# Kernel optimization log

Measured on AMD Instinct MI355X. Metric: run time of the kernel, lower is better.

## Reference

```python
import jax, jax.numpy as jnp
import numpy as np

NL, B, L1, L2, D = 4, 64, 256, 256, 1024
LOGIT_SCALE = 1.0
BN_EPS = 1e-8


def setup_inputs() -> dict:
    key = jax.random.key(0)
    k1, k2, k3, k4, k5, k6 = jax.random.split(key, 6)
    reps1 = jax.random.normal(k1, (NL, B, L1, D), dtype=jnp.float32)
    reps2 = jax.random.normal(k2, (NL, B, L2, D), dtype=jnp.float32)
    len1 = jax.random.randint(k3, (B,), 1, L1 + 1)
    len2 = jax.random.randint(k4, (B,), 1, L2 + 1)
    w = jax.random.normal(k5, (1, NL), dtype=jnp.float32) * 0.1
    b = jax.random.normal(k6, (1,), dtype=jnp.float32) * 0.1
    return {"reps1": reps1, "reps2": reps2, "len1": len1, "len2": len2, "w": w, "b": b}


def reference(reps1, reps2, len1, len2, w, b):
    # reps: (NL, B, L, D) hidden states of selected layers, already (B-major per layer)
    neg = jnp.finfo(reps1.dtype).min
    # cosine-normalize along feature dim
    h1 = reps1 / jnp.linalg.norm(reps1, axis=-1, keepdims=True)
    h2 = reps2 / jnp.linalg.norm(reps2, axis=-1, keepdims=True)
    # similarity matrices for all layers at once: (NL, B, L1, L2)
    dots = jnp.einsum("lbid,lbjd->lbij", h1, h2)
    # ragged validity masks
    mask1 = jnp.arange(L1)[None, :] < len1[:, None]  # (B, L1)
    mask2 = jnp.arange(L2)[None, :] < len2[:, None]  # (B, L2)
    n1 = len1.astype(dots.dtype)
    n2 = len2.astype(dots.dtype)
    # max over valid rows i, mean over valid cols j  -> s1 (NL, B)
    max_i = jnp.max(jnp.where(mask1[None, :, :, None], dots, neg), axis=2)  # (NL,B,L2)
    s1 = jnp.sum(jnp.where(mask2[None], max_i, 0.0), axis=2) / n2[None]
    # max over valid cols j, mean over valid rows i  -> s2 (NL, B)
    max_j = jnp.max(jnp.where(mask2[None, :, None, :], dots, neg), axis=3)  # (NL,B,L1)
    s2 = jnp.sum(jnp.where(mask1[None], max_j, 0.0), axis=2) / n1[None]
    # harmonic mean (F1)
    feat = (2.0 * s1 * s2 / (s1 + s2)).T  # (B, NL)
    # BatchNorm1d(affine=False), training mode: batch stats, biased variance
    mean = jnp.mean(feat, axis=0, keepdims=True)
    var = jnp.mean((feat - mean) ** 2, axis=0, keepdims=True)
    feat = (feat - mean) / jnp.sqrt(var + BN_EPS)
    # final linear head + logit scale -> (B,)
    return LOGIT_SCALE * (feat @ w.T + b)[:, 0]
```

## Files before the change

kernel.cpp:

```cpp
#include <hip/hip_runtime.h>

#define NLAYERS 4
#define BATCH   64
#define LEN1    256
#define LEN2    256
#define DIM     1024
#define BKK     32
#define NKT     (DIM / BKK)

typedef _Float16 f16x8 __attribute__((ext_vector_type(8)));
typedef float    f32x4 __attribute__((ext_vector_type(4)));

typedef __attribute__((address_space(1))) const void gas_void;
typedef __attribute__((address_space(3))) void       las_void;

__device__ __forceinline__ void dma16(const float* g, float* l) {
  __builtin_amdgcn_global_load_lds((gas_void*)g, (las_void*)l, 16, 0, 0);
}

__device__ __forceinline__ void block_bar() {
  asm volatile("" ::: "memory");
  __builtin_amdgcn_s_barrier();
  asm volatile("" ::: "memory");
}

#define WAITVM(N) asm volatile("s_waitcnt vmcnt(" #N ")" ::: "memory")

__global__ __launch_bounds__(1024, 4)
void bs_main(const float* __restrict__ reps1, const float* __restrict__ reps2,
             const int* __restrict__ len1, const int* __restrict__ len2,
             float* __restrict__ feat) {
  __shared__ float Af[2][LEN1 * BKK];
  __shared__ float Bf[2][LEN2 * BKK];
  __shared__ float ssq1[LEN1];
  __shared__ float ssq2[LEN2];
  __shared__ float rowp[LEN1][4];
  __shared__ float colp[LEN2][4];
  __shared__ float redbuf[32];

  const int bid = blockIdx.x;
  const int nl  = bid >> 6;
  const int bb  = bid & 63;
  const float* gA = reps1 + (size_t)bid * LEN1 * DIM;
  const float* gB = reps2 + (size_t)bid * LEN2 * DIM;

  const int tid  = threadIdx.x;
  const int lane = tid & 63;
  const int wid  = tid >> 6;
  const int wm   = wid >> 2;
  const int wn   = wid & 3;
  const int li   = lane & 15;
  const int lh   = lane >> 4;

  f32x4 acc[4][4];
  #pragma unroll
  for (int a = 0; a < 4; ++a)
    #pragma unroll
    for (int c = 0; c < 4; ++c) acc[a][c] = 0.0f;

  const int r0  = tid >> 3;
  const int ch0 = tid & 7;
  const int sc0 = (ch0 ^ (r0 & 7)) << 2;
  const int sc1 = (ch0 ^ ((r0 + 128) & 7)) << 2;

  float pssqA0 = 0.f, pssqA1 = 0.f, pssqB0 = 0.f, pssqB1 = 0.f;

  auto stage = [&](int kt, int buf) {
    const int col = kt * BKK;
    dma16(gA + (size_t)r0 * DIM + col + sc0,          &Af[buf][tid * 4]);
    dma16(gB + (size_t)r0 * DIM + col + sc0,          &Bf[buf][tid * 4]);
    dma16(gA + (size_t)(r0 + 128) * DIM + col + sc1,  &Af[buf][(tid + 1024) * 4]);
    dma16(gB + (size_t)(r0 + 128) * DIM + col + sc1,  &Bf[buf][(tid + 1024) * 4]);
  };

  stage(0, 0);

  #pragma unroll 1
  for (int kt = 0; kt < NKT; ++kt) {
    const int cur = kt & 1;
    if (kt + 1 < NKT) {
      stage(kt + 1, cur ^ 1);
      WAITVM(4);
    } else {
      WAITVM(0);
    }
    block_bar();

    const float* Ac = Af[cur];
    const float* Bc = Bf[cur];

    {
      const float4 a0 = *(const float4*)&Ac[tid * 4];
      const float4 a1 = *(const float4*)&Ac[(tid + 1024) * 4];
      const float4 b0 = *(const float4*)&Bc[tid * 4];
      const float4 b1 = *(const float4*)&Bc[(tid + 1024) * 4];
      pssqA0 += a0.x*a0.x + a0.y*a0.y + a0.z*a0.z + a0.w*a0.w;
      pssqA1 += a1.x*a1.x + a1.y*a1.y + a1.z*a1.z + a1.w*a1.w;
      pssqB0 += b0.x*b0.x + b0.y*b0.y + b0.z*b0.z + b0.w*b0.w;
      pssqB1 += b1.x*b1.x + b1.y*b1.y + b1.z*b1.z + b1.w*b1.w;
    }

    f16x8 af[4];
    #pragma unroll
    for (int fm = 0; fm < 4; ++fm) {
      const int r = wm * 64 + fm * 16 + li;
      const float4 x0 = *(const float4*)&Ac[r * BKK + ((((lh << 1)    ) ^ (r & 7)) << 2)];
      const float4 x1 = *(const float4*)&Ac[r * BKK + ((((lh << 1) | 1) ^ (r & 7)) << 2)];
      f16x8 h;
      h[0] = (_Float16)x0.x; h[1] = (_Float16)x0.y; h[2] = (_Float16)x0.z; h[3] = (_Float16)x0.w;
      h[4] = (_Float16)x1.x; h[5] = (_Float16)x1.y; h[6] = (_Float16)x1.z; h[7] = (_Float16)x1.w;
      af[fm] = h;
    }
    #pragma unroll
    for (int fn = 0; fn < 4; ++fn) {
      const int r = wn * 64 + fn * 16 + li;
      const float4 y0 = *(const float4*)&Bc[r * BKK + ((((lh << 1)    ) ^ (r & 7)) << 2)];
      const float4 y1 = *(const float4*)&Bc[r * BKK + ((((lh << 1) | 1) ^ (r & 7)) << 2)];
      f16x8 bh;
      bh[0] = (_Float16)y0.x; bh[1] = (_Float16)y0.y; bh[2] = (_Float16)y0.z; bh[3] = (_Float16)y0.w;
      bh[4] = (_Float16)y1.x; bh[5] = (_Float16)y1.y; bh[6] = (_Float16)y1.z; bh[7] = (_Float16)y1.w;
      #pragma unroll
      for (int fm = 0; fm < 4; ++fm)
        acc[fm][fn] = __builtin_amdgcn_mfma_f32_16x16x32_f16(af[fm], bh, acc[fm][fn], 0, 0, 0);
    }

    block_bar();
  }

  #pragma unroll
  for (int m = 1; m <= 4; m <<= 1) {
    pssqA0 += __shfl_xor(pssqA0, m, 64);
    pssqA1 += __shfl_xor(pssqA1, m, 64);
    pssqB0 += __shfl_xor(pssqB0, m, 64);
    pssqB1 += __shfl_xor(pssqB1, m, 64);
  }
  if ((lane & 7) == 0) {
    ssq1[r0] = pssqA0;  ssq1[r0 + 128] = pssqA1;
    ssq2[r0] = pssqB0;  ssq2[r0 + 128] = pssqB1;
  }
  __syncthreads();
  if (tid < 256)       ssq1[tid] = 1.0f / sqrtf(ssq1[tid]);
  else if (tid < 512)  ssq2[tid - 256] = 1.0f / sqrtf(ssq2[tid - 256]);
  __syncthreads();

  const int n1 = len1[bb];
  const int n2 = len2[bb];

  float rn2v[4];
  bool  jv[4];
  #pragma unroll
  for (int fn = 0; fn < 4; ++fn) {
    const int j = wn * 64 + fn * 16 + li;
    rn2v[fn] = ssq2[j];
    jv[fn]   = (j < n2);
  }
  float rn1v[4][4];
  bool  iv[4][4];
  #pragma unroll
  for (int fm = 0; fm < 4; ++fm)
    #pragma unroll
    for (int rg = 0; rg < 4; ++rg) {
      const int i = wm * 64 + fm * 16 + lh * 4 + rg;
      rn1v[fm][rg] = ssq1[i];
      iv[fm][rg]   = (i < n1);
    }

  const float NEG = -3.402823466e38f;
  float rowm[4][4];
  float colm[4];
  #pragma unroll
  for (int fm = 0; fm < 4; ++fm)
    #pragma unroll
    for (int rg = 0; rg < 4; ++rg) rowm[fm][rg] = NEG;
  #pragma unroll
  for (int fn = 0; fn < 4; ++fn) colm[fn] = NEG;

  #pragma unroll
  for (int fm = 0; fm < 4; ++fm)
    #pragma unroll
    for (int fn = 0; fn < 4; ++fn)
      #pragma unroll
      for (int rg = 0; rg < 4; ++rg) {
        const float v = acc[fm][fn][rg] * rn1v[fm][rg] * rn2v[fn];
        if (jv[fn] && v > rowm[fm][rg]) rowm[fm][rg] = v;
        if (iv[fm][rg] && v > colm[fn]) colm[fn] = v;
      }

  #pragma unroll
  for (int m = 1; m <= 8; m <<= 1)
    #pragma unroll
    for (int fm = 0; fm < 4; ++fm)
      #pragma unroll
      for (int rg = 0; rg < 4; ++rg) {
        const float o = __shfl_xor(rowm[fm][rg], m, 64);
        rowm[fm][rg] = fmaxf(rowm[fm][rg], o);
      }
  #pragma unroll
  for (int m = 16; m <= 32; m <<= 1)
    #pragma unroll
    for (int fn = 0; fn < 4; ++fn) {
      const float o = __shfl_xor(colm[fn], m, 64);
      colm[fn] = fmaxf(colm[fn], o);
    }

  if (li == 0)
    #pragma unroll
    for (int fm = 0; fm < 4; ++fm)
      #pragma unroll
      for (int rg = 0; rg < 4; ++rg)
        rowp[wm * 64 + fm * 16 + lh * 4 + rg][wn] = rowm[fm][rg];
  if (lh == 0)
    #pragma unroll
    for (int fn = 0; fn < 4; ++fn)
      colp[wn * 64 + fn * 16 + li][wm] = colm[fn];
  __syncthreads();

  float c1 = 0.f, c2 = 0.f;
  if (tid < 256) {
    const float rm = fmaxf(fmaxf(rowp[tid][0], rowp[tid][1]),
                           fmaxf(rowp[tid][2], rowp[tid][3]));
    if (tid < n1) c2 = rm;
    const float cm = fmaxf(fmaxf(colp[tid][0], colp[tid][1]),
                           fmaxf(colp[tid][2], colp[tid][3]));
    if (tid < n2) c1 = cm;
  }
  #pragma unroll
  for (int m = 1; m <= 32; m <<= 1) {
    c1 += __shfl_xor(c1, m, 64);
    c2 += __shfl_xor(c2, m, 64);
  }
  if (lane == 0) {
    redbuf[wid]      = c1;
    redbuf[16 + wid] = c2;
  }
  __syncthreads();
  if (tid == 0) {
    float s1s = 0.f, s2s = 0.f;
    #pragma unroll
    for (int i = 0; i < 16; ++i) { s1s += redbuf[i]; s2s += redbuf[16 + i]; }
    const float s1 = s1s / (float)n2;
    const float s2 = s2s / (float)n1;
    feat[bb * NLAYERS + nl] = 2.0f * s1 * s2 / (s1 + s2);
  }
}

__global__ void bs_head(const float* __restrict__ feat, const float* __restrict__ w,
                        const float* __restrict__ bias, float* __restrict__ out) {
  __shared__ float lds[NLAYERS][BATCH];
  const int tid = threadIdx.x;
  const int nl  = tid >> 6;
  const int b   = tid & 63;

  const float x = feat[b * NLAYERS + nl];
  float s = x;
  #pragma unroll
  for (int m = 1; m <= 32; m <<= 1) s += __shfl_xor(s, m, 64);
  const float mean = s / 64.0f;
  const float d = x - mean;
  float v = d * d;
  #pragma unroll
  for (int m = 1; m <= 32; m <<= 1) v += __shfl_xor(v, m, 64);
  const float var = v / 64.0f;
  const float y = d / sqrtf(var + 1e-8f);

  lds[nl][b] = y * w[nl];
  __syncthreads();
  if (tid < 64)
    out[tid] = lds[0][tid] + lds[1][tid] + lds[2][tid] + lds[3][tid] + bias[0];
}

extern "C" void kernel_launch(void* const* d_in, const int* in_sizes, int n_in,
                              void* d_out, int out_size, void* d_ws, size_t ws_size,
                              hipStream_t stream) {
  const float* reps1 = (const float*)d_in[0];
  const float* reps2 = (const float*)d_in[1];
  const int*   len1  = (const int*)d_in[2];
  const int*   len2  = (const int*)d_in[3];
  const float* w     = (const float*)d_in[4];
  const float* bias  = (const float*)d_in[5];
  float* feat = (float*)d_ws;

  bs_main<<<NLAYERS * BATCH, 1024, 0, stream>>>(reps1, reps2, len1, len2, feat);
  bs_head<<<1, 256, 0, stream>>>(feat, w, bias, (float*)d_out);
}
```

Baseline: 127.7 us.

## Use 4-stage pipeline with 16-wide K tiles and 16x16x16 MFMA

Halves the K tile width to 16, moves from double to quad buffering with three tiles in flight, and switches to the 16x16x16 f16 MFMA with 4-element fragments. Each thread now issues two DMA loads per stage instead of four, and the swizzle and sum-of-squares reduction are adapted to 4 chunks per row. The goal is deeper memory latency hiding at the same LDS footprint, at the cost of twice as many barriers and loop iterations and a lower-throughput MFMA variant.

Result: slower. 148.4 us (+16.2%).

```diff
diff --git a/kernel.cpp b/kernel.cpp
--- a/kernel.cpp
+++ b/kernel.cpp
@@ -5,10 +5,11 @@
 #define LEN1    256
 #define LEN2    256
 #define DIM     1024
-#define BKK     32
+#define BKK     16
 #define NKT     (DIM / BKK)
-
-typedef _Float16 f16x8 __attribute__((ext_vector_type(8)));
+#define NBUF    4
+
+typedef _Float16 f16x4 __attribute__((ext_vector_type(4)));
 typedef float    f32x4 __attribute__((ext_vector_type(4)));
 
 typedef __attribute__((address_space(1))) const void gas_void;
@@ -30,8 +31,8 @@
 void bs_main(const float* __restrict__ reps1, const float* __restrict__ reps2,
              const int* __restrict__ len1, const int* __restrict__ len2,
              float* __restrict__ feat) {
-  __shared__ float Af[2][LEN1 * BKK];
-  __shared__ float Bf[2][LEN2 * BKK];
+  __shared__ float Af[NBUF][LEN1 * BKK];
+  __shared__ float Bf[NBUF][LEN2 * BKK];
   __shared__ float ssq1[LEN1];
   __shared__ float ssq2[LEN2];
   __shared__ float rowp[LEN1][4];
@@ -58,32 +59,29 @@
     #pragma unroll
     for (int c = 0; c < 4; ++c) acc[a][c] = 0.0f;
 
-  const int r0  = tid >> 3;
-  const int ch0 = tid & 7;
-  const int sc0 = (ch0 ^ (r0 & 7)) << 2;
-  const int sc1 = (ch0 ^ ((r0 + 128) & 7)) << 2;
-
-  float pssqA0 = 0.f, pssqA1 = 0.f, pssqB0 = 0.f, pssqB1 = 0.f;
+  const int rS  = tid >> 2;
+  const int chS = tid & 3;
+  const int sc  = (chS ^ (rS & 3)) << 2;
+
+  float pssqA = 0.f, pssqB = 0.f;
 
   auto stage = [&](int kt, int buf) {
-    const int col = kt * BKK;
-    dma16(gA + (size_t)r0 * DIM + col + sc0,          &Af[buf][tid * 4]);
-    dma16(gB + (size_t)r0 * DIM + col + sc0,          &Bf[buf][tid * 4]);
-    dma16(gA + (size_t)(r0 + 128) * DIM + col + sc1,  &Af[buf][(tid + 1024) * 4]);
-    dma16(gB + (size_t)(r0 + 128) * DIM + col + sc1,  &Bf[buf][(tid + 1024) * 4]);
+    const int col = kt * BKK + sc;
+    dma16(gA + (size_t)rS * DIM + col, &Af[buf][tid * 4]);
+    dma16(gB + (size_t)rS * DIM + col, &Bf[buf][tid * 4]);
   };
 
   stage(0, 0);
+  stage(1, 1);
+  stage(2, 2);
 
   #pragma unroll 1
   for (int kt = 0; kt < NKT; ++kt) {
-    const int cur = kt & 1;
-    if (kt + 1 < NKT) {
-      stage(kt + 1, cur ^ 1);
-      WAITVM(4);
-    } else {
-      WAITVM(0);
-    }
+    const int cur = kt & (NBUF - 1);
+    if (kt + 3 < NKT) { stage(kt + 3, (kt + 3) & (NBUF - 1)); WAITVM(6); }
+    else if (kt + 2 < NKT) { WAITVM(4); }
+    else if (kt + 1 < NKT) { WAITVM(2); }
+    else { WAITVM(0); }
     block_bar();
 
     const float* Ac = Af[cur];
@@ -91,52 +89,43 @@
 
     {
       const float4 a0 = *(const float4*)&Ac[tid * 4];
-      const float4 a1 = *(const float4*)&Ac[(tid + 1024) * 4];
       const float4 b0 = *(const float4*)&Bc[tid * 4];
-      const float4 b1 = *(const float4*)&Bc[(tid + 1024) * 4];
-      pssqA0 += a0.x*a0.x + a0.y*a0.y + a0.z*a0.z + a0.w*a0.w;
-      pssqA1 += a1.x*a1.x + a1.y*a1.y + a1.z*a1.z + a1.w*a1.w;
-      pssqB0 += b0.x*b0.x + b0.y*b0.y + b0.z*b0.z + b0.w*b0.w;
-      pssqB1 += b1.x*b1.x + b1.y*b1.y + b1.z*b1.z + b1.w*b1.w;
-    }
-
-    f16x8 af[4];
+      pssqA += a0.x*a0.x + a0.y*a0.y + a0.z*a0.z + a0.w*a0.w;
+      pssqB += b0.x*b0.x + b0.y*b0.y + b0.z*b0.z + b0.w*b0.w;
+    }
+
+    f16x4 af[4];
     #pragma unroll
     for (int fm = 0; fm < 4; ++fm) {
       const int r = wm * 64 + fm * 16 + li;
-      const float4 x0 = *(const float4*)&Ac[r * BKK + ((((lh << 1)    ) ^ (r & 7)) << 2)];
-      const float4 x1 = *(const float4*)&Ac[r * BKK + ((((lh << 1) | 1) ^ (r & 7)) << 2)];
-      f16x8 h;
-      h[0] = (_Float16)x0.x; h[1] = (_Float16)x0.y; h[2] = (_Float16)x0.z; h[3] = (_Float16)x0.w;
-      h[4] = (_Float16)x1.x; h[5] = (_Float16)x1.y; h[6] = (_Float16)x1.z; h[7] = (_Float16)x1.w;
+      const float4 x = *(const float4*)&Ac[r * BKK + ((lh ^ (r & 3)) << 2)];
+      f16x4 h;
+      h[0] = (_Float16)x.x; h[1] = (_Float16)x.y;
+      h[2] = (_Float16)x.z; h[3] = (_Float16)x.w;
       af[fm] = h;
     }
     #pragma unroll
     for (int fn = 0; fn < 4; ++fn) {
       const int r = wn * 64 + fn * 16 + li;
-      const float4 y0 = *(const float4*)&Bc[r * BKK + ((((lh << 1)    ) ^ (r & 7)) << 2)];
-      const float4 y1 = *(const float4*)&Bc[r * BKK + ((((lh << 1) | 1) ^ (r & 7)) << 2)];
-      f16x8 bh;
-      bh[0] = (_Float16)y0.x; bh[1] = (_Float16)y0.y; bh[2] = (_Float16)y0.z; bh[3] = (_Float16)y0.w;
-      bh[4] = (_Float16)y1.x; bh[5] = (_Float16)y1.y; bh[6] = (_Float16)y1.z; bh[7] = (_Float16)y1.w;
+      const float4 y = *(const float4*)&Bc[r * BKK + ((lh ^ (r & 3)) << 2)];
+      f16x4 bh;
+      bh[0] = (_Float16)y.x; bh[1] = (_Float16)y.y;
+      bh[2] = (_Float16)y.z; bh[3] = (_Float16)y.w;
       #pragma unroll
       for (int fm = 0; fm < 4; ++fm)
-        acc[fm][fn] = __builtin_amdgcn_mfma_f32_16x16x32_f16(af[fm], bh, acc[fm][fn], 0, 0, 0);
+        acc[fm][fn] = __builtin_amdgcn_mfma_f32_16x16x16f16(af[fm], bh, acc[fm][fn], 0, 0, 0);
     }
 
     block_bar();
   }
 
-  #pragma unroll
-  for (int m = 1; m <= 4; m <<= 1) {
-    pssqA0 += __shfl_xor(pssqA0, m, 64);
-    pssqA1 += __shfl_xor(pssqA1, m, 64);
-    pssqB0 += __shfl_xor(pssqB0, m, 64);
-    pssqB1 += __shfl_xor(pssqB1, m, 64);
-  }
-  if ((lane & 7) == 0) {
-    ssq1[r0] = pssqA0;  ssq1[r0 + 128] = pssqA1;
-    ssq2[r0] = pssqB0;  ssq2[r0 + 128] = pssqB1;
+  pssqA += __shfl_xor(pssqA, 1, 64);
+  pssqA += __shfl_xor(pssqA, 2, 64);
+  pssqB += __shfl_xor(pssqB, 1, 64);
+  pssqB += __shfl_xor(pssqB, 2, 64);
+  if (chS == 0) {
+    ssq1[rS] = pssqA;
+    ssq2[rS] = pssqB;
   }
   __syncthreads();
   if (tid < 256)       ssq1[tid] = 1.0f / sqrtf(ssq1[tid]);
```
